# Performance work log

Hardware: AMD Instinct MI355X
Metric: run time of the kernel (lower is better)

## Reference

```python
import jax, jax.numpy as jnp
import numpy as np

# Module config (matches init_kwargs)
ANCHORS = np.array([[4.0, 4.0, 4.0], [8.0, 8.0, 8.0], [16.0, 16.0, 16.0]], dtype=np.float32)  # (w,h,d) per anchor
NUM_CLASSES = 1
IMG_SIZE = (96, 96, 96)  # (W, H, D)

B, A = 16, 3
ATTRS = 5 + NUM_CLASSES
D = H = W = 48


def setup_inputs() -> dict:
    key = jax.random.key(0)
    inp = jax.random.normal(key, (B, A * ATTRS, D, H, W), dtype=jnp.float32)
    return {"inp": inp}


def reference(inp):
    b, _, d, h, w = inp.shape
    stride_w = IMG_SIZE[0] / w
    stride_h = IMG_SIZE[1] / h
    stride_d = IMG_SIZE[2] / d

    # [B, A, D, H, W, attrs]
    pred = inp.reshape(b, A, ATTRS, d, h, w).transpose(0, 1, 3, 4, 5, 2)

    x = jax.nn.sigmoid(pred[..., 0])
    y = jax.nn.sigmoid(pred[..., 1])
    z = jax.nn.sigmoid(pred[..., 2])
    l = pred[..., 3]
    conf = jax.nn.sigmoid(pred[..., 4])
    pred_cls = jax.nn.sigmoid(pred[..., 5:])

    # Broadcast grids (replaces the nested python-loop fills)
    grid_x = jnp.arange(w, dtype=inp.dtype)                    # (W,) -> last axis
    grid_y = jnp.arange(h, dtype=inp.dtype)[:, None]           # (H,1)
    grid_z = jnp.arange(d, dtype=inp.dtype)[:, None, None]     # (D,1,1)

    # Original uses scaled anchor WIDTH for the length channel
    anchor_len = (jnp.asarray(ANCHORS[:, 0], dtype=inp.dtype) / stride_w)[None, :, None, None, None]

    bx = (x + grid_x) * stride_w
    by = (y + grid_y) * stride_h
    bz = (z + grid_z) * stride_d
    bl = jnp.exp(l) * anchor_len * stride_w

    boxes = jnp.stack([bx, by, bz, bl], axis=-1)  # [B,A,D,H,W,4]

    out = jnp.concatenate(
        [boxes.reshape(b, -1, 4), conf.reshape(b, -1, 1), pred_cls.reshape(b, -1, NUM_CLASSES)],
        axis=-1,
    )
    return out
```

## Files before the change

### kernel.cpp

```cpp
#include <hip/hip_runtime.h>


typedef float vf4 __attribute__((ext_vector_type(4)));

#define DHW    110592
#define HW48   2304
#define SPB    1024
#define BPP    108
#define F4B    1536
#define F4P    165888
#define CH4    27648
#define TPB    2
#define NBLK   2592

struct Frag { vf4 x, y, z, l, c, k; };

__device__ __forceinline__ float sigm(float v) {
    return 1.0f / (1.0f + __expf(-v));
}

__device__ __forceinline__ int swz(int i) {
    return (i & ~7) | ((i ^ (i >> 3)) & 7);
}

__device__ __forceinline__ void lds_barrier() {
    asm volatile("s_waitcnt lgkmcnt(0)" ::: "memory");
    __builtin_amdgcn_s_barrier();
}

__device__ __forceinline__ void load_frag(const float* __restrict__ in, int T,
                                          int tid, Frag& f) {
    const int p = T / BPP;
    const int chunk = T - p * BPP;
    const vf4* ip = (const vf4*)(in + (size_t)p * (6 * DHW) + chunk * SPB) + tid;
    f.x = __builtin_nontemporal_load(ip + 0 * CH4);
    f.y = __builtin_nontemporal_load(ip + 1 * CH4);
    f.z = __builtin_nontemporal_load(ip + 2 * CH4);
    f.l = __builtin_nontemporal_load(ip + 3 * CH4);
    f.c = __builtin_nontemporal_load(ip + 4 * CH4);
    f.k = __builtin_nontemporal_load(ip + 5 * CH4);
}

__device__ __forceinline__ void process(float* __restrict__ out, int T, int tid,
                                        const Frag& f, vf4* lds) {
    const int p = T / BPP;
    const int chunk = T - p * BPP;
    const int a = p % 3;
    const float anchw = (a == 0) ? 4.0f : (a == 1) ? 8.0f : 16.0f;
    const int S = chunk * SPB + tid * 4;
    const float xf = (float)(S % 48);
    const float yf = (float)((S / 48) % 48);
    const float zf = (float)(S / HW48);

    float bx[4], by[4], bz[4], bl[4], cf[4], cl[4];
#pragma unroll
    for (int q = 0; q < 4; ++q) {
        bx[q] = (sigm(f.x[q]) + xf + (float)q) * 2.0f;
        by[q] = (sigm(f.y[q]) + yf) * 2.0f;
        bz[q] = (sigm(f.z[q]) + zf) * 2.0f;
        bl[q] = __expf(f.l[q]) * anchw;
        cf[q] = sigm(f.c[q]);
        cl[q] = sigm(f.k[q]);
    }

    const int wb = 6 * tid;
    lds[swz(wb + 0)] = (vf4){bx[0], by[0], bz[0], bl[0]};
    lds[swz(wb + 1)] = (vf4){cf[0], cl[0], bx[1], by[1]};
    lds[swz(wb + 2)] = (vf4){bz[1], bl[1], cf[1], cl[1]};
    lds[swz(wb + 3)] = (vf4){bx[2], by[2], bz[2], bl[2]};
    lds[swz(wb + 4)] = (vf4){cf[2], cl[2], bx[3], by[3]};
    lds[swz(wb + 5)] = (vf4){bz[3], bl[3], cf[3], cl[3]};

    lds_barrier();

    vf4* op = (vf4*)out + (size_t)p * F4P + (size_t)chunk * F4B;
#pragma unroll
    for (int kk = 0; kk < 6; ++kk) {
        const int i = tid + 256 * kk;
        __builtin_nontemporal_store(lds[swz(i)], op + i);
    }

    lds_barrier();
}

__global__ __launch_bounds__(256) void DecodeBox_kernel(
    const float* __restrict__ in, float* __restrict__ out) {
    __shared__ vf4 lds[F4B];
    const int tid = threadIdx.x;
    const int T0 = blockIdx.x * TPB;

    Frag A, B;
    load_frag(in, T0, tid, A);
#pragma unroll
    for (int t = 0; t < TPB; ++t) {
        if (t + 1 < TPB) load_frag(in, T0 + t + 1, tid, B);
        process(out, T0 + t, tid, A, lds);
        A = B;
    }
}

extern "C" void kernel_launch(void* const* d_in, const int* in_sizes, int n_in,
                              void* d_out, int out_size, void* d_ws, size_t ws_size,
                              hipStream_t stream) {
    const float* in = (const float*)d_in[0];
    float* out = (float*)d_out;
    DecodeBox_kernel<<<NBLK, 256, 0, stream>>>(in, out);
}
```

Baseline: 212.8 us.

## Use per-wavefront LDS transpose regions to drop block barriers, double tiles per block

Each wavefront now owns a private 384-entry LDS region for the AoS transpose, so it only waits on its own LDS ops instead of two block-wide barriers per tile. Output stores are re-indexed per wave. Tiles per block go from 2 to 4, which halves the grid. Without a barrier, a wave's next-tile LDS writes could race with its own pending reads, so correctness relies on in-order execution within the wave. The larger tile count also reduces parallelism across blocks.

```diff
diff --git a/kernel.cpp b/kernel.cpp
--- a/kernel.cpp
+++ b/kernel.cpp
@@ -10,8 +10,9 @@
 #define F4B    1536
 #define F4P    165888
 #define CH4    27648
-#define TPB    2
-#define NBLK   2592
+#define TPB    4
+#define NBLK   1296
+#define WREG   384
 
 struct Frag { vf4 x, y, z, l, c, k; };
 
@@ -21,11 +22,6 @@
 
 __device__ __forceinline__ int swz(int i) {
     return (i & ~7) | ((i ^ (i >> 3)) & 7);
-}
-
-__device__ __forceinline__ void lds_barrier() {
-    asm volatile("s_waitcnt lgkmcnt(0)" ::: "memory");
-    __builtin_amdgcn_s_barrier();
 }
 
 __device__ __forceinline__ void load_frag(const float* __restrict__ in, int T,
@@ -42,7 +38,7 @@
 }
 
 __device__ __forceinline__ void process(float* __restrict__ out, int T, int tid,
-                                        const Frag& f, vf4* lds) {
+                                        const Frag& f, vf4* __restrict__ wlds) {
     const int p = T / BPP;
     const int chunk = T - p * BPP;
     const int a = p % 3;
@@ -63,30 +59,30 @@
         cl[q] = sigm(f.k[q]);
     }
 
-    const int wb = 6 * tid;
-    lds[swz(wb + 0)] = (vf4){bx[0], by[0], bz[0], bl[0]};
-    lds[swz(wb + 1)] = (vf4){cf[0], cl[0], bx[1], by[1]};
-    lds[swz(wb + 2)] = (vf4){bz[1], bl[1], cf[1], cl[1]};
-    lds[swz(wb + 3)] = (vf4){bx[2], by[2], bz[2], bl[2]};
-    lds[swz(wb + 4)] = (vf4){cf[2], cl[2], bx[3], by[3]};
-    lds[swz(wb + 5)] = (vf4){bz[3], bl[3], cf[3], cl[3]};
+    const int lane = tid & 63;
+    const int wb = 6 * lane;
+    wlds[swz(wb + 0)] = (vf4){bx[0], by[0], bz[0], bl[0]};
+    wlds[swz(wb + 1)] = (vf4){cf[0], cl[0], bx[1], by[1]};
+    wlds[swz(wb + 2)] = (vf4){bz[1], bl[1], cf[1], cl[1]};
+    wlds[swz(wb + 3)] = (vf4){bx[2], by[2], bz[2], bl[2]};
+    wlds[swz(wb + 4)] = (vf4){cf[2], cl[2], bx[3], by[3]};
+    wlds[swz(wb + 5)] = (vf4){bz[3], bl[3], cf[3], cl[3]};
 
-    lds_barrier();
+    asm volatile("s_waitcnt lgkmcnt(0)" ::: "memory");
 
-    vf4* op = (vf4*)out + (size_t)p * F4P + (size_t)chunk * F4B;
+    vf4* op = (vf4*)out + (size_t)p * F4P + (size_t)chunk * F4B + (tid >> 6) * WREG;
 #pragma unroll
     for (int kk = 0; kk < 6; ++kk) {
-        const int i = tid + 256 * kk;
-        __builtin_nontemporal_store(lds[swz(i)], op + i);
+        const int i = lane + 64 * kk;
+        __builtin_nontemporal_store(wlds[swz(i)], op + i);
     }
-
-    lds_barrier();
 }
 
 __global__ __launch_bounds__(256) void DecodeBox_kernel(
     const float* __restrict__ in, float* __restrict__ out) {
     __shared__ vf4 lds[F4B];
     const int tid = threadIdx.x;
+    vf4* wlds = lds + (tid >> 6) * WREG;
     const int T0 = blockIdx.x * TPB;
 
     Frag A, B;
@@ -94,7 +90,7 @@
 #pragma unroll
     for (int t = 0; t < TPB; ++t) {
         if (t + 1 < TPB) load_frag(in, T0 + t + 1, tid, B);
-        process(out, T0 + t, tid, A, lds);
+        process(out, T0 + t, tid, A, wlds);
         A = B;
     }
 }
```

Result: slower. 218.5 us (+2.7%).
